# Kernel optimization log

Hardware: AMD Instinct MI355X
Metric: run time of the kernel (lower is better)

## Reference

```python
import jax, jax.numpy as jnp
import numpy as np

S, B, H = 2048, 1, 1024
N_HEADS = 16
HEAD_DIM = H // N_HEADS
E, K, F = 8, 2, 2048  # experts, top_k, ffn_hidden
EPS = 1e-5


def layernorm(x, w, b):
    mu = jnp.mean(x, axis=-1, keepdims=True)
    var = jnp.mean(jnp.square(x - mu), axis=-1, keepdims=True)
    return (x - mu) * jax.lax.rsqrt(var + EPS) * w + b


def setup_inputs() -> dict:
    key = jax.random.key(0)
    ks = jax.random.split(key, 8)
    std = 0.02
    return {
        "x": jax.random.normal(ks[0], (S, B, H), dtype=jnp.float32),
        "ln1_w": jnp.ones((H,), jnp.float32),
        "ln1_b": jnp.zeros((H,), jnp.float32),
        "in_proj_w": jax.random.normal(ks[1], (3 * H, H), jnp.float32) * std,
        "in_proj_b": jnp.zeros((3 * H,), jnp.float32),
        "out_proj_w": jax.random.normal(ks[2], (H, H), jnp.float32) * std,
        "out_proj_b": jnp.zeros((H,), jnp.float32),
        "ln2_w": jnp.ones((H,), jnp.float32),
        "ln2_b": jnp.zeros((H,), jnp.float32),
        "router_w": jax.random.normal(ks[3], (E, H), jnp.float32) * std,
        "w1": jax.random.normal(ks[4], (E, H, F), jnp.float32) * std,
        "w2": jax.random.normal(ks[5], (E, F, H), jnp.float32) * std,
    }


def reference(x, ln1_w, ln1_b, in_proj_w, in_proj_b, out_proj_w, out_proj_b,
              ln2_w, ln2_b, router_w, w1, w2):
    s, b, h = x.shape
    # ---- causal self-attention (nn.MultiheadAttention math) ----
    hn = layernorm(x, ln1_w, ln1_b)
    qkv = hn @ in_proj_w.T + in_proj_b          # [S,B,3H]
    q, k, v = jnp.split(qkv, 3, axis=-1)
    q = q.reshape(s, b, N_HEADS, HEAD_DIM)
    k = k.reshape(s, b, N_HEADS, HEAD_DIM)
    v = v.reshape(s, b, N_HEADS, HEAD_DIM)
    scores = jnp.einsum('sbnd,tbnd->bnst', q, k) / np.sqrt(HEAD_DIM)
    causal = jnp.tril(jnp.ones((s, s), bool))
    scores = jnp.where(causal[None, None], scores, -jnp.inf)
    probs = jax.nn.softmax(scores, axis=-1)
    attn = jnp.einsum('bnst,tbnd->sbnd', probs, v).reshape(s, b, h)
    attn = attn @ out_proj_w.T + out_proj_b
    x1 = x + attn
    # ---- dMoE FFN: router softmax -> top-k gates -> expert GELU MLP ----
    hn2 = layernorm(x1, ln2_w, ln2_b).reshape(s * b, h)   # tokens [T,H]
    logits = hn2 @ router_w.T                              # [T,E]
    rp = jax.nn.softmax(logits, axis=-1)
    topw, topi = jax.lax.top_k(rp, K)                      # [T,K]
    gates = jnp.sum(jax.nn.one_hot(topi, E, dtype=hn2.dtype) * topw[..., None], axis=1)  # [T,E]
    hmid = jax.nn.gelu(jnp.einsum('th,ehf->tef', hn2, w1), approximate=False)  # [T,E,F]
    y = jnp.einsum('tef,efh->th', hmid * gates[:, :, None], w2)                # [T,H]
    return x1 + y.reshape(s, b, h)
```

## Files before the change

### kernel.cpp

```cpp
#include <hip/hip_runtime.h>

#define SL 2048
#define HID 1024
#define NHEAD 16
#define HD 64
#define NEXP 8
#define FF 2048
#define MAXTILE 40
#define MAXROWS (MAXTILE * 128)
#define CPAD 32
#define BPITCH 36

typedef short bf16x8 __attribute__((ext_vector_type(8)));
typedef float f32x4 __attribute__((ext_vector_type(4)));
typedef unsigned u32x4 __attribute__((ext_vector_type(4)));

__device__ __forceinline__ unsigned short f2bf(float f) {
  unsigned u = __builtin_bit_cast(unsigned, f);
  u += 0x7fffu + ((u >> 16) & 1u);
  return (unsigned short)(u >> 16);
}

__device__ __forceinline__ void gload16(const void* g, void* l) {
  __builtin_amdgcn_global_load_lds((const __attribute__((address_space(1))) void*)g,
                                   (__attribute__((address_space(3))) void*)l,
                                   16, 0, 0);
}

__device__ __forceinline__ void xcd_remap(int& bx, int& by) {
  const int nx = gridDim.x;
  const int nwg = nx * gridDim.y;
  const int L = by * nx + bx;
  const int per = nwg >> 3;
  const int Lp = (L & 7) * per + (L >> 3);
  bx = Lp % nx;
  by = Lp / nx;
}

#define PIPE_WAIT(i, NT)                                                     \
  if ((i) == (NT) - 1)                                                       \
    asm volatile("s_waitcnt vmcnt(0) lgkmcnt(0)" ::: "memory");              \
  else                                                                       \
    asm volatile("s_waitcnt vmcnt(4) lgkmcnt(0)" ::: "memory");              \
  __builtin_amdgcn_s_barrier();

#define GEMM_FRAGS_MFMA(CC)                                                  \
  bf16x8 af[4], bfr[4];                                                      \
  _Pragma("unroll")                                                          \
  for (int mt = 0; mt < 4; mt++)                                             \
    af[mt] = *reinterpret_cast<const bf16x8*>(                               \
        &Asm[CC][(wm + mt * 16 + la) * 32 + lk]);                            \
  _Pragma("unroll")                                                          \
  for (int nt = 0; nt < 4; nt++)                                             \
    bfr[nt] = *reinterpret_cast<const bf16x8*>(                              \
        &Bsm[CC][(wn + nt * 16 + la) * 32 + lk]);                            \
  __builtin_amdgcn_s_setprio(1);                                             \
  _Pragma("unroll")                                                          \
  for (int mt = 0; mt < 4; mt++)                                             \
    _Pragma("unroll")                                                        \
    for (int nt = 0; nt < 4; nt++)                                           \
      acc[mt][nt] =                                                          \
          __builtin_amdgcn_mfma_f32_16x16x32_bf16(af[mt], bfr[nt], acc[mt][nt], 0, 0, 0); \
  __builtin_amdgcn_s_setprio(0);

#define PIPE_ROT()                                                           \
  cc = (cc == 2) ? 0 : cc + 1;                                               \
  cs = (cs == 2) ? 0 : cs + 1;

template <int MODE>
__global__ __launch_bounds__(256) void gemm_bt(
    const unsigned short* __restrict__ A, const unsigned short* __restrict__ Bt,
    int M, int N, int Kstride, int Kloop,
    const float* __restrict__ bias,
    float* __restrict__ outf,
    unsigned short* __restrict__ q_out, unsigned short* __restrict__ k_out,
    unsigned short* __restrict__ vt_out)
{
  __shared__ unsigned short Asm[3][128 * 32];
  __shared__ unsigned short Bsm[3][128 * 32];
  int bx = blockIdx.x, by = blockIdx.y;
  xcd_remap(bx, by);
  const int tid = threadIdx.x;
  const int wave = tid >> 6;
  const int lane = tid & 63;
  const int m0 = by * 128;
  const int n0 = bx * 128;
  const int koff = blockIdx.z * Kloop;
  const int wm = (wave >> 1) * 64;
  const int wn = (wave & 1) * 64;
  const int la = lane & 15;
  const int lk = (lane >> 4) * 8;

  f32x4 acc[4][4] = {};

  const int srow = tid >> 2;
  const int skoff = (tid & 3) * 8;
  const unsigned short* Ag = A + (size_t)(m0 + srow) * Kstride + koff + skoff;
  const unsigned short* Bg = Bt + (size_t)(n0 + srow) * Kstride + koff + skoff;

  auto stage = [&](int s, int k0) {
    gload16(Ag + k0, &Asm[s][wave * 512]);
    gload16(Ag + (size_t)64 * Kstride + k0, &Asm[s][2048 + wave * 512]);
    gload16(Bg + k0, &Bsm[s][wave * 512]);
    gload16(Bg + (size_t)64 * Kstride + k0, &Bsm[s][2048 + wave * 512]);
  };

  stage(0, 0);
  stage(1, 32);
  const int NT = Kloop >> 5;
  int cc = 0, cs = 2;
  for (int i = 0; i < NT; ++i) {
    PIPE_WAIT(i, NT)
    if (i + 2 < NT) stage(cs, (i + 2) << 5);
    GEMM_FRAGS_MFMA(cc)
    PIPE_ROT()
  }

  const int lg = lane >> 4;
#pragma unroll
  for (int mt = 0; mt < 4; mt++) {
#pragma unroll
    for (int nt = 0; nt < 4; nt++) {
#pragma unroll
      for (int r = 0; r < 4; r++) {
        const int row = m0 + wm + mt * 16 + lg * 4 + r;
        const int col = n0 + wn + nt * 16 + la;
        float v = acc[mt][nt][r];
        if (MODE == 0) {
          v += bias[col];
          const int hh = (col & 1023) >> 6;
          const int dd = col & 63;
          const unsigned short bv = f2bf(v);
          if (col < 1024)
            q_out[(size_t)hh * SL * HD + (size_t)row * HD + dd] = bv;
          else if (col < 2048)
            k_out[(size_t)hh * SL * HD + (size_t)row * HD + dd] = bv;
          else
            vt_out[(size_t)hh * HD * SL + (size_t)dd * SL + row] = bv;
        } else {
          outf[(size_t)blockIdx.z * SL * HID + (size_t)row * HID + col] = v;
        }
      }
    }
  }
}


__device__ __forceinline__ bf16x8 bfragB(const unsigned short* Bu, int n, int lk) {
  const uint2 lo = *reinterpret_cast<const uint2*>(&Bu[n * BPITCH + lk]);
  const uint2 hi = *reinterpret_cast<const uint2*>(&Bu[n * BPITCH + lk + 4]);
  u32x4 w; w[0] = lo.x; w[1] = lo.y; w[2] = hi.x; w[3] = hi.y;
  return __builtin_bit_cast(bf16x8, w);
}

#define MOE_FRAGS_MFMA(CC)                                                   \
  bf16x8 af[4], bfr[4];                                                      \
  _Pragma("unroll")                                                          \
  for (int mt = 0; mt < 4; mt++)                                             \
    af[mt] = *reinterpret_cast<const bf16x8*>(                               \
        &Asm[CC][(wm + mt * 16 + la) * 32 + lk]);                            \
  _Pragma("unroll")                                                          \
  for (int nt = 0; nt < 4; nt++)                                             \
    bfr[nt] = bfragB(BsmU[CC], wn + nt * 16 + la, lk);                       \
  __builtin_amdgcn_s_setprio(1);                                             \
  _Pragma("unroll")                                                          \
  for (int mt = 0; mt < 4; mt++)                                             \
    _Pragma("unroll")                                                        \
    for (int nt = 0; nt < 4; nt++)                                           \
      acc[mt][nt] =                                                          \
          __builtin_amdgcn_mfma_f32_16x16x32_bf16(af[mt], bfr[nt], acc[mt][nt], 0, 0, 0); \
  __builtin_amdgcn_s_setprio(0);

__global__ __launch_bounds__(256) void gemm_moe1(
    const unsigned short* __restrict__ A, const float* __restrict__ w1,
    const int* __restrict__ perm, const float* __restrict__ gateg,
    const int* __restrict__ texp, const int* __restrict__ trow,
    unsigned short* __restrict__ hmidg)
{
  __shared__ unsigned short Asm[2][128 * 32];
  __shared__ unsigned short BsmU[2][128 * BPITCH];
  int bx = blockIdx.x, by = blockIdx.y;
  xcd_remap(bx, by);
  const int e = texp[by];
  if (e < 0) return;
  const int row0 = trow[by];
  const int tid = threadIdx.x;
  const int wave = tid >> 6;
  const int lane = tid & 63;
  const int n0 = bx * 128;
  const int wm = (wave >> 1) * 64;
  const int wn = (wave & 1) * 64;
  const int la = lane & 15;
  const int lk = (lane >> 4) * 8;
  f32x4 acc[4][4] = {};

  const int srow = tid >> 2;
  const int skoff = (tid & 3) * 8;
  const int p0 = perm[row0 + srow];
  const int p1 = perm[row0 + 64 + srow];
  const unsigned short* Ag0 = A + (size_t)(p0 < 0 ? 0 : (p0 >> 1)) * HID + skoff;
  const unsigned short* Ag1 = A + (size_t)(p1 < 0 ? 0 : (p1 >> 1)) * HID + skoff;
  const float* Bf = w1 + (size_t)e * HID * FF + n0;
  const int sc = tid & 31;
  const int skr = tid >> 5;

  auto stageA = [&](int buf, int k0) {
    gload16(Ag0 + k0, &Asm[buf][wave * 512]);
    gload16(Ag1 + k0, &Asm[buf][2048 + wave * 512]);
  };
  auto stageB = [&](int buf, int k0) {
#pragma unroll
    for (int p = 0; p < 4; p++) {
      const int k = p * 8 + skr;
      const float* src = Bf + (size_t)(k0 + k) * FF + sc;
#pragma unroll
      for (int j = 0; j < 4; j++)
        BsmU[buf][(sc + 32 * j) * BPITCH + k] = f2bf(src[32 * j]);
    }
  };

  stageA(0, 0);
  stageB(0, 0);
  __syncthreads();
  int cur = 0;
  for (int k0 = 0; k0 < HID; k0 += 32) {
    if (k0 + 32 < HID) {
      stageA(cur ^ 1, k0 + 32);
      stageB(cur ^ 1, k0 + 32);
    }
    MOE_FRAGS_MFMA(cur)
    __syncthreads();
    cur ^= 1;
  }

  const int lg = lane >> 4;
#pragma unroll
  for (int mt = 0; mt < 4; mt++) {
    float gr[4];
#pragma unroll
    for (int r = 0; r < 4; r++) gr[r] = gateg[row0 + wm + mt * 16 + lg * 4 + r];
#pragma unroll
    for (int nt = 0; nt < 4; nt++) {
#pragma unroll
      for (int r = 0; r < 4; r++) {
        const int grow = row0 + wm + mt * 16 + lg * 4 + r;
        const int col = n0 + wn + nt * 16 + la;
        const float v = acc[mt][nt][r];
        const float g = 0.5f * v * (1.0f + erff(v * 0.70710678118f));
        hmidg[(size_t)grow * FF + col] = f2bf(g * gr[r]);
      }
    }
  }
}

__global__ __launch_bounds__(256) void gemm_moe2(
    const unsigned short* __restrict__ A, const float* __restrict__ w2,
    const int* __restrict__ perm,
    const int* __restrict__ texp, const int* __restrict__ trow,
    float* __restrict__ ybuf)
{
  __shared__ unsigned short Asm[2][128 * 32];
  __shared__ unsigned short BsmU[2][128 * BPITCH];
  int bx = blockIdx.x, by = blockIdx.y;
  xcd_remap(bx, by);
  const int e = texp[by];
  if (e < 0) return;
  const int row0 = trow[by];
  const int tid = threadIdx.x;
  const int wave = tid >> 6;
  const int lane = tid & 63;
  const int n0 = bx * 128;
  const int koff = blockIdx.z * (FF / 2);
  const int wm = (wave >> 1) * 64;
  const int wn = (wave & 1) * 64;
  const int la = lane & 15;
  const int lk = (lane >> 4) * 8;
  f32x4 acc[4][4] = {};

  const int srow = tid >> 2;
  const int skoff = (tid & 3) * 8;
  const unsigned short* Ag = A + (size_t)(row0 + srow) * FF + koff + skoff;
  const float* Bf = w2 + (size_t)e * FF * HID + (size_t)koff * HID + n0;
  const int sc = tid & 31;
  const int skr = tid >> 5;

  auto stageA = [&](int buf, int k0) {
    gload16(Ag + k0, &Asm[buf][wave * 512]);
    gload16(Ag + (size_t)64 * FF + k0, &Asm[buf][2048 + wave * 512]);
  };
  auto stageB = [&](int buf, int k0) {
#pragma unroll
    for (int p = 0; p < 4; p++) {
      const int k = p * 8 + skr;
      const float* src = Bf + (size_t)(k0 + k) * HID + sc;
#pragma unroll
      for (int j = 0; j < 4; j++)
        BsmU[buf][(sc + 32 * j) * BPITCH + k] = f2bf(src[32 * j]);
    }
  };

  stageA(0, 0);
  stageB(0, 0);
  __syncthreads();
  int cur = 0;
  for (int k0 = 0; k0 < FF / 2; k0 += 32) {
    if (k0 + 32 < FF / 2) {
      stageA(cur ^ 1, k0 + 32);
      stageB(cur ^ 1, k0 + 32);
    }
    MOE_FRAGS_MFMA(cur)
    __syncthreads();
    cur ^= 1;
  }

  const int lg = lane >> 4;
#pragma unroll
  for (int mt = 0; mt < 4; mt++) {
    int pr[4];
#pragma unroll
    for (int r = 0; r < 4; r++) pr[r] = perm[row0 + wm + mt * 16 + lg * 4 + r];
#pragma unroll
    for (int nt = 0; nt < 4; nt++) {
#pragma unroll
      for (int r = 0; r < 4; r++) {
        const int p = pr[r];
        if (p >= 0) {
          const int col = n0 + wn + nt * 16 + la;
          ybuf[(size_t)(blockIdx.z * 2 + (p & 1)) * SL * HID + (size_t)(p >> 1) * HID + col] =
              acc[mt][nt][r];
        }
      }
    }
  }
}

__global__ __launch_bounds__(256) void ln_kernel(
    const float* __restrict__ x, const float* __restrict__ w, const float* __restrict__ b,
    unsigned short* __restrict__ ob)
{
  const int row = blockIdx.x;
  const int tid = threadIdx.x;
  const float4 v = *reinterpret_cast<const float4*>(&x[(size_t)row * HID + tid * 4]);
  float s = v.x + v.y + v.z + v.w;
  float q = v.x * v.x + v.y * v.y + v.z * v.z + v.w * v.w;
  for (int off = 32; off > 0; off >>= 1) {
    s += __shfl_down(s, off);
    q += __shfl_down(q, off);
  }
  __shared__ float ps[4], pq[4];
  const int wave = tid >> 6, lane = tid & 63;
  if (lane == 0) { ps[wave] = s; pq[wave] = q; }
  __syncthreads();
  s = ps[0] + ps[1] + ps[2] + ps[3];
  q = pq[0] + pq[1] + pq[2] + pq[3];
  const float mu = s * (1.0f / HID);
  const float inv = rsqrtf(q * (1.0f / HID) - mu * mu + 1e-5f);
  const int i = tid * 4;
  const float4 wv = *reinterpret_cast<const float4*>(&w[i]);
  const float4 bv = *reinterpret_cast<const float4*>(&b[i]);
  ushort4 u;
  u.x = f2bf((v.x - mu) * inv * wv.x + bv.x);
  u.y = f2bf((v.y - mu) * inv * wv.y + bv.y);
  u.z = f2bf((v.z - mu) * inv * wv.z + bv.z);
  u.w = f2bf((v.w - mu) * inv * wv.w + bv.w);
  *reinterpret_cast<ushort4*>(&ob[(size_t)row * HID + i]) = u;
}

__global__ __launch_bounds__(256) void combine_ln(
    const float4* __restrict__ x, const float* __restrict__ bias,
    const float4* __restrict__ p0, const float4* __restrict__ p1,
    float4* __restrict__ x1,
    const float* __restrict__ w, const float* __restrict__ b,
    unsigned short* __restrict__ ob, float* __restrict__ of)
{
  const int row = blockIdx.x;
  const int tid = threadIdx.x;
  const int i4 = row * 256 + tid;
  const int i = tid * 4;
  const float4 bv0 = *reinterpret_cast<const float4*>(&bias[i]);
  const float4 a = x[i4], c = p0[i4], d = p1[i4];
  float4 v;
  v.x = a.x + bv0.x + c.x + d.x;
  v.y = a.y + bv0.y + c.y + d.y;
  v.z = a.z + bv0.z + c.z + d.z;
  v.w = a.w + bv0.w + c.w + d.w;
  x1[i4] = v;
  float s = v.x + v.y + v.z + v.w;
  float q = v.x * v.x + v.y * v.y + v.z * v.z + v.w * v.w;
  for (int off = 32; off > 0; off >>= 1) {
    s += __shfl_down(s, off);
    q += __shfl_down(q, off);
  }
  __shared__ float ps[4], pq[4];
  const int wave = tid >> 6, lane = tid & 63;
  if (lane == 0) { ps[wave] = s; pq[wave] = q; }
  __syncthreads();
  s = ps[0] + ps[1] + ps[2] + ps[3];
  q = pq[0] + pq[1] + pq[2] + pq[3];
  const float mu = s * (1.0f / HID);
  const float inv = rsqrtf(q * (1.0f / HID) - mu * mu + 1e-5f);
  const float4 wv = *reinterpret_cast<const float4*>(&w[i]);
  const float4 bv = *reinterpret_cast<const float4*>(&b[i]);
  const float o0 = (v.x - mu) * inv * wv.x + bv.x;
  const float o1 = (v.y - mu) * inv * wv.y + bv.y;
  const float o2 = (v.z - mu) * inv * wv.z + bv.z;
  const float o3 = (v.w - mu) * inv * wv.w + bv.w;
  ushort4 u; u.x = f2bf(o0); u.y = f2bf(o1); u.z = f2bf(o2); u.w = f2bf(o3);
  *reinterpret_cast<ushort4*>(&ob[(size_t)row * HID + i]) = u;
  float4 o; o.x = o0; o.y = o1; o.z = o2; o.w = o3;
  *reinterpret_cast<float4*>(&of[(size_t)row * HID + i]) = o;
}

__global__ __launch_bounds__(256) void conv_bf16_2(
    const float4* __restrict__ a, const float4* __restrict__ b,
    ushort4* __restrict__ oa, ushort4* __restrict__ ob, int na4, int nb4)
{
  const int i = blockIdx.x * 256 + threadIdx.x;
  if (i < na4) {
    const float4 v = a[i];
    ushort4 u; u.x = f2bf(v.x); u.y = f2bf(v.y); u.z = f2bf(v.z); u.w = f2bf(v.w);
    oa[i] = u;
  } else if (i - na4 < nb4) {
    const float4 v = b[i - na4];
    ushort4 u; u.x = f2bf(v.x); u.y = f2bf(v.y); u.z = f2bf(v.z); u.w = f2bf(v.w);
    ob[i - na4] = u;
  }
}

__global__ __launch_bounds__(256) void router_kernel(
    const float* __restrict__ hn2f, const float* __restrict__ rw,
    int* __restrict__ ti, float* __restrict__ tg, int* __restrict__ cnt)
{
  __shared__ float wlds[NEXP * HID];
  __shared__ int lcnt[NEXP];
  const int tid = threadIdx.x;
#pragma unroll
  for (int i = 0; i < 8; i++)
    *reinterpret_cast<float4*>(&wlds[i * 1024 + tid * 4]) =
        *reinterpret_cast<const float4*>(&rw[i * 1024 + tid * 4]);
  if (tid < NEXP) lcnt[tid] = 0;
  __syncthreads();

  const int wave = tid >> 6, lane = tid & 63;
#pragma unroll 1
  for (int k = 0; k < 4; k++) {
    const int t = blockIdx.x * 16 + wave * 4 + k;
    float4 xr[4];
#pragma unroll
    for (int c = 0; c < 4; c++)
      xr[c] = *reinterpret_cast<const float4*>(&hn2f[(size_t)t * HID + c * 256 + lane * 4]);
    float p[NEXP];
#pragma unroll
    for (int e = 0; e < NEXP; e++) {
      float s = 0.f;
#pragma unroll
      for (int c = 0; c < 4; c++) {
        const float4 wv = *reinterpret_cast<const float4*>(&wlds[e * 1024 + c * 256 + lane * 4]);
        s += xr[c].x * wv.x + xr[c].y * wv.y + xr[c].z * wv.z + xr[c].w * wv.w;
      }
      s += __shfl_xor(s, 32);
      s += __shfl_xor(s, 16);
      s += __shfl_xor(s, 8);
      s += __shfl_xor(s, 4);
      s += __shfl_xor(s, 2);
      s += __shfl_xor(s, 1);
      p[e] = s;
    }
    if (lane == 0) {
      float mx = p[0];
#pragma unroll
      for (int e = 1; e < NEXP; e++) mx = fmaxf(mx, p[e]);
      float Z = 0.f;
#pragma unroll
      for (int e = 0; e < NEXP; e++) { p[e] = expf(p[e] - mx); Z += p[e]; }
      const float invZ = 1.f / Z;
      int i1 = 0;
#pragma unroll
      for (int e = 1; e < NEXP; e++) if (p[e] > p[i1]) i1 = e;
      int i2 = (i1 == 0) ? 1 : 0;
#pragma unroll
      for (int e = 0; e < NEXP; e++) if (e != i1 && p[e] > p[i2]) i2 = e;
      ti[2 * t] = i1; ti[2 * t + 1] = i2;
      tg[2 * t] = p[i1] * invZ; tg[2 * t + 1] = p[i2] * invZ;
      atomicAdd(&lcnt[i1], 1);
      atomicAdd(&lcnt[i2], 1);
    }
  }
  __syncthreads();
  if (tid < NEXP && lcnt[tid] > 0) atomicAdd(&cnt[tid * CPAD], lcnt[tid]);
}

__global__ void scan_kernel(const int* __restrict__ cnt, int* __restrict__ poff,
                            int* __restrict__ texp, int* __restrict__ trow)
{
  if (threadIdx.x == 0 && blockIdx.x == 0) {
    int off = 0, nt = 0;
    for (int e = 0; e < NEXP; e++) {
      poff[e] = off;
      const int c = cnt[e * CPAD];
      const int ntl = (c + 127) >> 7;
      for (int i = 0; i < ntl; i++) { texp[nt] = e; trow[nt] = off + i * 128; nt++; }
      off += ntl * 128;
    }
    for (int i = nt; i < MAXTILE; i++) { texp[i] = -1; trow[i] = 0; }
  }
}

__global__ __launch_bounds__(256) void build_kernel(
    const int* __restrict__ ti, const float* __restrict__ tg,
    const int* __restrict__ poff, int* __restrict__ fill,
    int* __restrict__ perm, float* __restrict__ gateg)
{
  __shared__ int lcnt[NEXP], lbase[NEXP];
  const int tid = threadIdx.x;
  if (tid < NEXP) lcnt[tid] = 0;
  __syncthreads();
  const int t = blockIdx.x * 256 + tid;
  int e0 = ti[2 * t], e1 = ti[2 * t + 1];
  int l0 = atomicAdd(&lcnt[e0], 1);
  int l1 = atomicAdd(&lcnt[e1], 1);
  __syncthreads();
  if (tid < NEXP) lbase[tid] = (lcnt[tid] > 0) ? atomicAdd(&fill[tid * CPAD], lcnt[tid]) : 0;
  __syncthreads();
  int pos0 = poff[e0] + lbase[e0] + l0;
  int pos1 = poff[e1] + lbase[e1] + l1;
  perm[pos0] = 2 * t;
  gateg[pos0] = tg[2 * t];
  perm[pos1] = 2 * t + 1;
  gateg[pos1] = tg[2 * t + 1];
}

__global__ __launch_bounds__(256) void final_add(
    const float4* __restrict__ x1, const float4* __restrict__ y0,
    const float4* __restrict__ y1, const float4* __restrict__ y2,
    const float4* __restrict__ y3, float4* __restrict__ out)
{
  const int i = blockIdx.x * 256 + threadIdx.x;
  const float4 a = x1[i], b = y0[i], c = y1[i], d = y2[i], e = y3[i];
  float4 o;
  o.x = a.x + b.x + c.x + d.x + e.x;
  o.y = a.y + b.y + c.y + d.y + e.y;
  o.z = a.z + b.z + c.z + d.z + e.z;
  o.w = a.w + b.w + c.w + d.w + e.w;
  out[i] = o;
}

#define SC2 0.1803368801111204f
#define PPITCH 20
__global__ __launch_bounds__(512) void attn_kernel(
    const unsigned short* __restrict__ qb, const unsigned short* __restrict__ kb,
    const unsigned short* __restrict__ vtb, unsigned short* __restrict__ attn)
{
  const int h = blockIdx.y;
  const int tid = threadIdx.x;
  const int wave = tid >> 6, lane = tid & 63;
  const int grp = wave >> 2;
  const int w4 = wave & 3;
  const int la = lane & 15, lg = lane >> 4;
  const int la7 = la & 7;
  __shared__ unsigned short Kt[2][2][64 * 64];
  __shared__ unsigned short Vt[2][2][64 * 64];
  __shared__ unsigned plds[8 * 32 * PPITCH];
  const unsigned short* qh = qb + (size_t)h * SL * HD;
  const unsigned short* kh = kb + (size_t)h * SL * HD;
  const unsigned short* vh = vtb + (size_t)h * HD * SL;
  unsigned* pu = &plds[wave * 32 * PPITCH];

  const int sr_lo = w4 * 8 + (lane >> 3);
  const int ss = lane & 7;

  auto stageKV = [&](int t, int buf) {
    const int kvb = t * 64;
#pragma unroll
    for (int j = 0; j < 2; j++) {
      const int row = j * 32 + sr_lo;
      const int s = ss ^ (row & 7);
      gload16(kh + (size_t)(kvb + row) * HD + s * 8, &Kt[grp][buf][j * 2048 + w4 * 512]);
      gload16(vh + (size_t)row * SL + kvb + s * 8, &Vt[grp][buf][j * 2048 + w4 * 512]);
    }
  };

  for (int half = 0; half < 2; half++) {
    const int qt = half ? (31 - blockIdx.x) : blockIdx.x;
    const int m0 = qt * 64 + w4 * 16;
    const int T = qt + 1;
    const int S = (T + 1) >> 1;
    const int q = m0 + la;

    bf16x8 aq0 = *reinterpret_cast<const bf16x8*>(&qh[(size_t)(m0 + la) * HD + lg * 8]);
    bf16x8 aq1 = *reinterpret_cast<const bf16x8*>(&qh[(size_t)(m0 + la) * HD + 32 + lg * 8]);

    f32x4 oacc[4] = {};
    float mrun = -1e30f, lrun = 0.f;

    if (grp < T) stageKV(grp, 0);
    __syncthreads();
    int cur = 0;

    for (int s = 0; s < S; s++) {
      const int tmy = 2 * s + grp;
      if (tmy + 2 < T) stageKV(tmy + 2, cur ^ 1);
      if (tmy < T) {
        const int kv0 = tmy * 64;
        const unsigned short* Kb = Kt[grp][cur];
        const unsigned short* Vb = Vt[grp][cur];

        f32x4 sac[4] = {};
        __builtin_amdgcn_s_setprio(1);
#pragma unroll
        for (int nt = 0; nt < 4; nt++) {
          const int row = nt * 16 + la;
          bf16x8 b0 = *reinterpret_cast<const bf16x8*>(&Kb[row * 64 + ((lg ^ la7) << 3)]);
          bf16x8 b1 = *reinterpret_cast<const bf16x8*>(&Kb[row * 64 + (((4 + lg) ^ la7) << 3)]);
          sac[nt] = __builtin_amdgcn_mfma_f32_16x16x32_bf16(b0, aq0, sac[nt], 0, 0, 0);
          sac[nt] = __builtin_amdgcn_mfma_f32_16x16x32_bf16(b1, aq1, sac[nt], 0, 0, 0);
        }
        __builtin_amdgcn_s_setprio(0);
        float sv[4][4];
        const bool diag = (tmy == qt);
#pragma unroll
        for (int nt = 0; nt < 4; nt++)
#pragma unroll
          for (int r = 0; r < 4; r++) {
            float xs = sac[nt][r] * SC2;
            if (diag && (kv0 + nt * 16 + lg * 4 + r) > q) xs = -1e30f;
            sv[nt][r] = xs;
          }
        float pm = fmaxf(fmaxf(sv[0][0], sv[0][1]), fmaxf(sv[0][2], sv[0][3]));
#pragma unroll
        for (int nt = 1; nt < 4; nt++)
          pm = fmaxf(pm, fmaxf(fmaxf(sv[nt][0], sv[nt][1]), fmaxf(sv[nt][2], sv[nt][3])));
        pm = fmaxf(pm, __shfl_xor(pm, 16));
        pm = fmaxf(pm, __shfl_xor(pm, 32));
        const float mn = fmaxf(mrun, pm);
        float rs = 0.f;
#pragma unroll
        for (int nt = 0; nt < 4; nt++)
#pragma unroll
          for (int r = 0; r < 4; r++) {
            const float pe = exp2f(sv[nt][r] - mn);
            sv[nt][r] = pe;
            rs += pe;
          }
        rs += __shfl_xor(rs, 16);
        rs += __shfl_xor(rs, 32);
        if (__ballot(pm > mrun) != 0ULL) {
          const float al = exp2f(mrun - mn);
#pragma unroll
          for (int dt = 0; dt < 4; dt++)
#pragma unroll
            for (int r = 0; r < 4; r++) oacc[dt][r] *= al;
          lrun = lrun * al + rs;
          mrun = mn;
        } else {
          lrun += rs;
        }
#pragma unroll
        for (int nt = 0; nt < 4; nt++)
#pragma unroll
          for (int rp = 0; rp < 2; rp++) {
            unsigned pk;
            asm("v_cvt_pk_bf16_f32 %0, %1, %2"
                : "=v"(pk) : "v"(sv[nt][rp * 2]), "v"(sv[nt][rp * 2 + 1]));
            pu[(nt * 8 + lg * 2 + rp) * PPITCH + la] = pk;
          }
        asm volatile("s_waitcnt lgkmcnt(0)" ::: "memory");
        __builtin_amdgcn_sched_barrier(0);
        u32x4 w0, w1;
#pragma unroll
        for (int jj = 0; jj < 4; jj++) {
          w0[jj] = pu[(lg * 4 + jj) * PPITCH + la];
          w1[jj] = pu[(16 + lg * 4 + jj) * PPITCH + la];
        }
        const bf16x8 pa0 = __builtin_bit_cast(bf16x8, w0);
        const bf16x8 pa1 = __builtin_bit_cast(bf16x8, w1);
        __builtin_amdgcn_s_setprio(1);
#pragma unroll
        for (int dt = 0; dt < 4; dt++) {
          const int row = dt * 16 + la;
          bf16x8 v0 = *reinterpret_cast<const bf16x8*>(&Vb[row * 64 + ((lg ^ la7) << 3)]);
          bf16x8 v1 = *reinterpret_cast<const bf16x8*>(&Vb[row * 64 + (((4 + lg) ^ la7) << 3)]);
          oacc[dt] = __builtin_amdgcn_mfma_f32_16x16x32_bf16(v0, pa0, oacc[dt], 0, 0, 0);
          oacc[dt] = __builtin_amdgcn_mfma_f32_16x16x32_bf16(v1, pa1, oacc[dt], 0, 0, 0);
        }
        __builtin_amdgcn_s_setprio(0);
      }
      __syncthreads();
      cur ^= 1;
    }

    float* xb = (float*)&Kt[0][0][0];
    float* mlb = (float*)&Vt[0][0][0];
    if (grp == 1) {
#pragma unroll
      for (int dt = 0; dt < 4; dt++)
#pragma unroll
        for (int r = 0; r < 4; r++)
          xb[w4 * 1024 + (dt * 16 + lg * 4 + r) * 16 + la] = oacc[dt][r];
      if (lg == 0) {
        mlb[w4 * 32 + la * 2] = mrun;
        mlb[w4 * 32 + la * 2 + 1] = lrun;
      }
    }
    __syncthreads();
    if (grp == 0) {
      const float m1 = mlb[w4 * 32 + la * 2];
      const float l1 = mlb[w4 * 32 + la * 2 + 1];
      const float mm = fmaxf(mrun, m1);
      const float a0 = exp2f(mrun - mm);
      const float a1 = exp2f(m1 - mm);
      const float linv = 1.0f / (lrun * a0 + l1 * a1);
#pragma unroll
      for (int dt = 0; dt < 4; dt++) {
        ushort4 u;
        float o0 = (oacc[dt][0] * a0 + xb[w4 * 1024 + (dt * 16 + lg * 4 + 0) * 16 + la] * a1) * linv;
        float o1 = (oacc[dt][1] * a0 + xb[w4 * 1024 + (dt * 16 + lg * 4 + 1) * 16 + la] * a1) * linv;
        float o2 = (oacc[dt][2] * a0 + xb[w4 * 1024 + (dt * 16 + lg * 4 + 2) * 16 + la] * a1) * linv;
        float o3 = (oacc[dt][3] * a0 + xb[w4 * 1024 + (dt * 16 + lg * 4 + 3) * 16 + la] * a1) * linv;
        u.x = f2bf(o0); u.y = f2bf(o1); u.z = f2bf(o2); u.w = f2bf(o3);
        *reinterpret_cast<ushort4*>(&attn[(size_t)q * HID + h * HD + dt * 16 + lg * 4]) = u;
      }
    }
    __syncthreads();
  }
}

extern "C" void kernel_launch(void* const* d_in, const int* in_sizes, int n_in,
                              void* d_out, int out_size, void* d_ws, size_t ws_size,
                              hipStream_t stream)
{
  const float* x          = (const float*)d_in[0];
  const float* ln1_w      = (const float*)d_in[1];
  const float* ln1_b      = (const float*)d_in[2];
  const float* in_proj_w  = (const float*)d_in[3];
  const float* in_proj_b  = (const float*)d_in[4];
  const float* out_proj_w = (const float*)d_in[5];
  const float* out_proj_b = (const float*)d_in[6];
  const float* ln2_w      = (const float*)d_in[7];
  const float* ln2_b      = (const float*)d_in[8];
  const float* router_w   = (const float*)d_in[9];
  const float* w1         = (const float*)d_in[10];
  const float* w2         = (const float*)d_in[11];
  float* out = (float*)d_out;

  char* ws = (char*)d_ws;
  size_t off = 0;
  auto alloc = [&](size_t bytes) -> void* {
    void* p = ws + off;
    off += (bytes + 255) & ~(size_t)255;
    return p;
  };
  unsigned short* hn_b   = (unsigned short*)alloc((size_t)SL * HID * 2);
  unsigned short* ipw_b  = (unsigned short*)alloc((size_t)3 * HID * HID * 2);
  unsigned short* opw_b  = (unsigned short*)alloc((size_t)HID * HID * 2);
  unsigned short* qb     = (unsigned short*)alloc((size_t)SL * HID * 2);
  unsigned short* kb     = (unsigned short*)alloc((size_t)SL * HID * 2);
  unsigned short* vtb    = (unsigned short*)alloc((size_t)SL * HID * 2);
  unsigned short* attn_b = (unsigned short*)alloc((size_t)SL * HID * 2);
  float*          x1     = (float*)alloc((size_t)SL * HID * 4);
  float*          pbuf   = (float*)alloc((size_t)2 * SL * HID * 4);
  unsigned short* hn2_b  = (unsigned short*)alloc((size_t)SL * HID * 2);
  float*          hn2_f  = (float*)alloc((size_t)SL * HID * 4);
  unsigned short* hmidg  = (unsigned short*)alloc((size_t)MAXROWS * FF * 2);
  float*          ybuf   = (float*)alloc((size_t)4 * SL * HID * 4);
  int*            ti     = (int*)alloc((size_t)SL * 2 * 4);
  float*          tg     = (float*)alloc((size_t)SL * 2 * 4);
  int*            perm   = (int*)alloc((size_t)MAXROWS * 4);
  float*          gateg  = (float*)alloc((size_t)MAXROWS * 4);
  int*            cnt    = (int*)alloc(NEXP * CPAD * 4);
  int*            fill   = (int*)alloc(NEXP * CPAD * 4);
  int*            poff   = (int*)alloc(64 * 4);
  int*            texp   = (int*)alloc(64 * 4);
  int*            trow   = (int*)alloc(64 * 4);

  const dim3 blk(256);

  hipMemsetAsync(cnt, 0, NEXP * CPAD * 4, stream);
  hipMemsetAsync(fill, 0, NEXP * CPAD * 4, stream);
  hipMemsetAsync(perm, 0xFF, (size_t)MAXROWS * 4, stream);
  hipMemsetAsync(gateg, 0, (size_t)MAXROWS * 4, stream);

  conv_bf16_2<<<4096, blk, 0, stream>>>(
      (const float4*)in_proj_w, (const float4*)out_proj_w,
      (ushort4*)ipw_b, (ushort4*)opw_b, 3 * HID * HID / 4, HID * HID / 4);

  ln_kernel<<<SL, blk, 0, stream>>>(x, ln1_w, ln1_b, hn_b);

  gemm_bt<0><<<dim3(3 * HID / 128, SL / 128), blk, 0, stream>>>(
      hn_b, ipw_b, SL, 3 * HID, HID, HID,
      in_proj_b, nullptr, qb, kb, vtb);

  attn_kernel<<<dim3(16, NHEAD), dim3(512), 0, stream>>>(qb, kb, vtb, attn_b);

  gemm_bt<2><<<dim3(HID / 128, SL / 128, 2), blk, 0, stream>>>(
      attn_b, opw_b, SL, HID, HID, HID / 2,
      nullptr, pbuf, nullptr, nullptr, nullptr);

  combine_ln<<<SL, blk, 0, stream>>>(
      (const float4*)x, out_proj_b, (const float4*)pbuf,
      (const float4*)(pbuf + (size_t)SL * HID), (float4*)x1,
      ln2_w, ln2_b, hn2_b, hn2_f);

  router_kernel<<<SL / 16, blk, 0, stream>>>(hn2_f, router_w, ti, tg, cnt);
  scan_kernel<<<1, 64, 0, stream>>>(cnt, poff, texp, trow);
  build_kernel<<<SL / 256, blk, 0, stream>>>(ti, tg, poff, fill, perm, gateg);

  gemm_moe1<<<dim3(FF / 128, MAXTILE), blk, 0, stream>>>(
      hn2_b, w1, perm, gateg, texp, trow, hmidg);
  gemm_moe2<<<dim3(HID / 128, MAXTILE, 2), blk, 0, stream>>>(
      hmidg, w2, perm, texp, trow, ybuf);

  final_add<<<SL * HID / 1024, blk, 0, stream>>>(
      (const float4*)x1, (const float4*)ybuf,
      (const float4*)(ybuf + (size_t)SL * HID),
      (const float4*)(ybuf + (size_t)2 * SL * HID),
      (const float4*)(ybuf + (size_t)3 * SL * HID),
      (float4*)out);
}
```

Before: 261.2 us.

## Register-prefetch MoE weight tiles and give each attention block one query tile

Both MoE GEMM kernels now load the next fp32 weight tile into registers before the MFMA work and only convert and write it to LDS afterwards. This overlaps global-load latency with compute, at the cost of 16 extra registers and a full vmcnt wait. The attention kernel drops its two-query-tiles-per-block pairing and launches 32 blocks per head with one tile each, heaviest first. That doubles the block count for more parallelism but gives up the paired load balancing.

```diff
diff --git a/kernel.cpp b/kernel.cpp
--- a/kernel.cpp
+++ b/kernel.cpp
@@ -145,7 +145,6 @@
   }
 }
 
-
 __device__ __forceinline__ bf16x8 bfragB(const unsigned short* Bu, int n, int lk) {
   const uint2 lo = *reinterpret_cast<const uint2*>(&Bu[n * BPITCH + lk]);
   const uint2 hi = *reinterpret_cast<const uint2*>(&Bu[n * BPITCH + lk + 4]);
@@ -204,31 +203,44 @@
   const int sc = tid & 31;
   const int skr = tid >> 5;
 
+  float brg[16];
+
   auto stageA = [&](int buf, int k0) {
     gload16(Ag0 + k0, &Asm[buf][wave * 512]);
     gload16(Ag1 + k0, &Asm[buf][2048 + wave * 512]);
   };
-  auto stageB = [&](int buf, int k0) {
+  auto loadB = [&](int k0) {
+#pragma unroll
+    for (int p = 0; p < 4; p++) {
+      const float* src = Bf + (size_t)(k0 + p * 8 + skr) * FF + sc;
+#pragma unroll
+      for (int j = 0; j < 4; j++) brg[p * 4 + j] = src[32 * j];
+    }
+  };
+  auto writeB = [&](int buf) {
 #pragma unroll
     for (int p = 0; p < 4; p++) {
       const int k = p * 8 + skr;
-      const float* src = Bf + (size_t)(k0 + k) * FF + sc;
 #pragma unroll
       for (int j = 0; j < 4; j++)
-        BsmU[buf][(sc + 32 * j) * BPITCH + k] = f2bf(src[32 * j]);
+        BsmU[buf][(sc + 32 * j) * BPITCH + k] = f2bf(brg[p * 4 + j]);
     }
   };
 
+  loadB(0);
   stageA(0, 0);
-  stageB(0, 0);
+  asm volatile("s_waitcnt vmcnt(0)" ::: "memory");
+  writeB(0);
   __syncthreads();
   int cur = 0;
   for (int k0 = 0; k0 < HID; k0 += 32) {
-    if (k0 + 32 < HID) {
-      stageA(cur ^ 1, k0 + 32);
-      stageB(cur ^ 1, k0 + 32);
-    }
+    const bool nx = (k0 + 32 < HID);
+    if (nx) { loadB(k0 + 32); stageA(cur ^ 1, k0 + 32); }
     MOE_FRAGS_MFMA(cur)
+    if (nx) {
+      asm volatile("s_waitcnt vmcnt(0)" ::: "memory");
+      writeB(cur ^ 1);
+    }
     __syncthreads();
     cur ^= 1;
   }
@@ -284,31 +296,44 @@
   const int sc = tid & 31;
   const int skr = tid >> 5;
 
+  float brg[16];
+
   auto stageA = [&](int buf, int k0) {
     gload16(Ag + k0, &Asm[buf][wave * 512]);
     gload16(Ag + (size_t)64 * FF + k0, &Asm[buf][2048 + wave * 512]);
   };
-  auto stageB = [&](int buf, int k0) {
+  auto loadB = [&](int k0) {
+#pragma unroll
+    for (int p = 0; p < 4; p++) {
+      const float* src = Bf + (size_t)(k0 + p * 8 + skr) * HID + sc;
+#pragma unroll
+      for (int j = 0; j < 4; j++) brg[p * 4 + j] = src[32 * j];
+    }
+  };
+  auto writeB = [&](int buf) {
 #pragma unroll
     for (int p = 0; p < 4; p++) {
       const int k = p * 8 + skr;
-      const float* src = Bf + (size_t)(k0 + k) * HID + sc;
 #pragma unroll
       for (int j = 0; j < 4; j++)
-        BsmU[buf][(sc + 32 * j) * BPITCH + k] = f2bf(src[32 * j]);
+        BsmU[buf][(sc + 32 * j) * BPITCH + k] = f2bf(brg[p * 4 + j]);
     }
   };
 
+  loadB(0);
   stageA(0, 0);
-  stageB(0, 0);
+  asm volatile("s_waitcnt vmcnt(0)" ::: "memory");
+  writeB(0);
   __syncthreads();
   int cur = 0;
   for (int k0 = 0; k0 < FF / 2; k0 += 32) {
-    if (k0 + 32 < FF / 2) {
-      stageA(cur ^ 1, k0 + 32);
-      stageB(cur ^ 1, k0 + 32);
-    }
+    const bool nx = (k0 + 32 < FF / 2);
+    if (nx) { loadB(k0 + 32); stageA(cur ^ 1, k0 + 32); }
     MOE_FRAGS_MFMA(cur)
+    if (nx) {
+      asm volatile("s_waitcnt vmcnt(0)" ::: "memory");
+      writeB(cur ^ 1);
+    }
     __syncthreads();
     cur ^= 1;
   }
@@ -580,148 +605,145 @@
     }
   };
 
-  for (int half = 0; half < 2; half++) {
-    const int qt = half ? (31 - blockIdx.x) : blockIdx.x;
-    const int m0 = qt * 64 + w4 * 16;
-    const int T = qt + 1;
-    const int S = (T + 1) >> 1;
-    const int q = m0 + la;
-
-    bf16x8 aq0 = *reinterpret_cast<const bf16x8*>(&qh[(size_t)(m0 + la) * HD + lg * 8]);
-    bf16x8 aq1 = *reinterpret_cast<const bf16x8*>(&qh[(size_t)(m0 + la) * HD + 32 + lg * 8]);
-
-    f32x4 oacc[4] = {};
-    float mrun = -1e30f, lrun = 0.f;
-
-    if (grp < T) stageKV(grp, 0);
+  const int qt = 31 - (int)blockIdx.x;
+  const int m0 = qt * 64 + w4 * 16;
+  const int T = qt + 1;
+  const int S = (T + 1) >> 1;
+  const int q = m0 + la;
+
+  bf16x8 aq0 = *reinterpret_cast<const bf16x8*>(&qh[(size_t)(m0 + la) * HD + lg * 8]);
+  bf16x8 aq1 = *reinterpret_cast<const bf16x8*>(&qh[(size_t)(m0 + la) * HD + 32 + lg * 8]);
+
+  f32x4 oacc[4] = {};
+  float mrun = -1e30f, lrun = 0.f;
+
+  if (grp < T) stageKV(grp, 0);
+  __syncthreads();
+  int cur = 0;
+
+  for (int s = 0; s < S; s++) {
+    const int tmy = 2 * s + grp;
+    if (tmy + 2 < T) stageKV(tmy + 2, cur ^ 1);
+    if (tmy < T) {
+      const int kv0 = tmy * 64;
+      const unsigned short* Kb = Kt[grp][cur];
+      const unsigned short* Vb = Vt[grp][cur];
+
+      f32x4 sac[4] = {};
+      __builtin_amdgcn_s_setprio(1);
+#pragma unroll
+      for (int nt = 0; nt < 4; nt++) {
+        const int row = nt * 16 + la;
+        bf16x8 b0 = *reinterpret_cast<const bf16x8*>(&Kb[row * 64 + ((lg ^ la7) << 3)]);
+        bf16x8 b1 = *reinterpret_cast<const bf16x8*>(&Kb[row * 64 + (((4 + lg) ^ la7) << 3)]);
+        sac[nt] = __builtin_amdgcn_mfma_f32_16x16x32_bf16(b0, aq0, sac[nt], 0, 0, 0);
+        sac[nt] = __builtin_amdgcn_mfma_f32_16x16x32_bf16(b1, aq1, sac[nt], 0, 0, 0);
+      }
+      __builtin_amdgcn_s_setprio(0);
+      float sv[4][4];
+      const bool diag = (tmy == qt);
+#pragma unroll
+      for (int nt = 0; nt < 4; nt++)
+#pragma unroll
+        for (int r = 0; r < 4; r++) {
+          float xs = sac[nt][r] * SC2;
+          if (diag && (kv0 + nt * 16 + lg * 4 + r) > q) xs = -1e30f;
+          sv[nt][r] = xs;
+        }
+      float pm = fmaxf(fmaxf(sv[0][0], sv[0][1]), fmaxf(sv[0][2], sv[0][3]));
+#pragma unroll
+      for (int nt = 1; nt < 4; nt++)
+        pm = fmaxf(pm, fmaxf(fmaxf(sv[nt][0], sv[nt][1]), fmaxf(sv[nt][2], sv[nt][3])));
+      pm = fmaxf(pm, __shfl_xor(pm, 16));
+      pm = fmaxf(pm, __shfl_xor(pm, 32));
+      const float mn = fmaxf(mrun, pm);
+      float rs = 0.f;
+#pragma unroll
+      for (int nt = 0; nt < 4; nt++)
+#pragma unroll
+        for (int r = 0; r < 4; r++) {
+          const float pe = exp2f(sv[nt][r] - mn);
+          sv[nt][r] = pe;
+          rs += pe;
+        }
+      rs += __shfl_xor(rs, 16);
+      rs += __shfl_xor(rs, 32);
+      if (__ballot(pm > mrun) != 0ULL) {
+        const float al = exp2f(mrun - mn);
+#pragma unroll
+        for (int dt = 0; dt < 4; dt++)
+#pragma unroll
+          for (int r = 0; r < 4; r++) oacc[dt][r] *= al;
+        lrun = lrun * al + rs;
+        mrun = mn;
+      } else {
+        lrun += rs;
+      }
+#pragma unroll
+      for (int nt = 0; nt < 4; nt++)
+#pragma unroll
+        for (int rp = 0; rp < 2; rp++) {
+          unsigned pk;
+          asm("v_cvt_pk_bf16_f32 %0, %1, %2"
+              : "=v"(pk) : "v"(sv[nt][rp * 2]), "v"(sv[nt][rp * 2 + 1]));
+          pu[(nt * 8 + lg * 2 + rp) * PPITCH + la] = pk;
+        }
+      asm volatile("s_waitcnt lgkmcnt(0)" ::: "memory");
+      __builtin_amdgcn_sched_barrier(0);
+      u32x4 w0, w1;
+#pragma unroll
+      for (int jj = 0; jj < 4; jj++) {
+        w0[jj] = pu[(lg * 4 + jj) * PPITCH + la];
+        w1[jj] = pu[(16 + lg * 4 + jj) * PPITCH + la];
+      }
+      const bf16x8 pa0 = __builtin_bit_cast(bf16x8, w0);
+      const bf16x8 pa1 = __builtin_bit_cast(bf16x8, w1);
+      __builtin_amdgcn_s_setprio(1);
+#pragma unroll
+      for (int dt = 0; dt < 4; dt++) {
+        const int row = dt * 16 + la;
+        bf16x8 v0 = *reinterpret_cast<const bf16x8*>(&Vb[row * 64 + ((lg ^ la7) << 3)]);
+        bf16x8 v1 = *reinterpret_cast<const bf16x8*>(&Vb[row * 64 + (((4 + lg) ^ la7) << 3)]);
+        oacc[dt] = __builtin_amdgcn_mfma_f32_16x16x32_bf16(v0, pa0, oacc[dt], 0, 0, 0);
+        oacc[dt] = __builtin_amdgcn_mfma_f32_16x16x32_bf16(v1, pa1, oacc[dt], 0, 0, 0);
+      }
+      __builtin_amdgcn_s_setprio(0);
+    }
     __syncthreads();
-    int cur = 0;
-
-    for (int s = 0; s < S; s++) {
-      const int tmy = 2 * s + grp;
-      if (tmy + 2 < T) stageKV(tmy + 2, cur ^ 1);
-      if (tmy < T) {
-        const int kv0 = tmy * 64;
-        const unsigned short* Kb = Kt[grp][cur];
-        const unsigned short* Vb = Vt[grp][cur];
-
-        f32x4 sac[4] = {};
-        __builtin_amdgcn_s_setprio(1);
-#pragma unroll
-        for (int nt = 0; nt < 4; nt++) {
-          const int row = nt * 16 + la;
-          bf16x8 b0 = *reinterpret_cast<const bf16x8*>(&Kb[row * 64 + ((lg ^ la7) << 3)]);
-          bf16x8 b1 = *reinterpret_cast<const bf16x8*>(&Kb[row * 64 + (((4 + lg) ^ la7) << 3)]);
-          sac[nt] = __builtin_amdgcn_mfma_f32_16x16x32_bf16(b0, aq0, sac[nt], 0, 0, 0);
-          sac[nt] = __builtin_amdgcn_mfma_f32_16x16x32_bf16(b1, aq1, sac[nt], 0, 0, 0);
-        }
-        __builtin_amdgcn_s_setprio(0);
-        float sv[4][4];
-        const bool diag = (tmy == qt);
-#pragma unroll
-        for (int nt = 0; nt < 4; nt++)
-#pragma unroll
-          for (int r = 0; r < 4; r++) {
-            float xs = sac[nt][r] * SC2;
-            if (diag && (kv0 + nt * 16 + lg * 4 + r) > q) xs = -1e30f;
-            sv[nt][r] = xs;
-          }
-        float pm = fmaxf(fmaxf(sv[0][0], sv[0][1]), fmaxf(sv[0][2], sv[0][3]));
-#pragma unroll
-        for (int nt = 1; nt < 4; nt++)
-          pm = fmaxf(pm, fmaxf(fmaxf(sv[nt][0], sv[nt][1]), fmaxf(sv[nt][2], sv[nt][3])));
-        pm = fmaxf(pm, __shfl_xor(pm, 16));
-        pm = fmaxf(pm, __shfl_xor(pm, 32));
-        const float mn = fmaxf(mrun, pm);
-        float rs = 0.f;
-#pragma unroll
-        for (int nt = 0; nt < 4; nt++)
-#pragma unroll
-          for (int r = 0; r < 4; r++) {
-            const float pe = exp2f(sv[nt][r] - mn);
-            sv[nt][r] = pe;
-            rs += pe;
-          }
-        rs += __shfl_xor(rs, 16);
-        rs += __shfl_xor(rs, 32);
-        if (__ballot(pm > mrun) != 0ULL) {
-          const float al = exp2f(mrun - mn);
-#pragma unroll
-          for (int dt = 0; dt < 4; dt++)
-#pragma unroll
-            for (int r = 0; r < 4; r++) oacc[dt][r] *= al;
-          lrun = lrun * al + rs;
-          mrun = mn;
-        } else {
-          lrun += rs;
-        }
-#pragma unroll
-        for (int nt = 0; nt < 4; nt++)
-#pragma unroll
-          for (int rp = 0; rp < 2; rp++) {
-            unsigned pk;
-            asm("v_cvt_pk_bf16_f32 %0, %1, %2"
-                : "=v"(pk) : "v"(sv[nt][rp * 2]), "v"(sv[nt][rp * 2 + 1]));
-            pu[(nt * 8 + lg * 2 + rp) * PPITCH + la] = pk;
-          }
-        asm volatile("s_waitcnt lgkmcnt(0)" ::: "memory");
-        __builtin_amdgcn_sched_barrier(0);
-        u32x4 w0, w1;
-#pragma unroll
-        for (int jj = 0; jj < 4; jj++) {
-          w0[jj] = pu[(lg * 4 + jj) * PPITCH + la];
-          w1[jj] = pu[(16 + lg * 4 + jj) * PPITCH + la];
-        }
-        const bf16x8 pa0 = __builtin_bit_cast(bf16x8, w0);
-        const bf16x8 pa1 = __builtin_bit_cast(bf16x8, w1);
-        __builtin_amdgcn_s_setprio(1);
-#pragma unroll
-        for (int dt = 0; dt < 4; dt++) {
-          const int row = dt * 16 + la;
-          bf16x8 v0 = *reinterpret_cast<const bf16x8*>(&Vb[row * 64 + ((lg ^ la7) << 3)]);
-          bf16x8 v1 = *reinterpret_cast<const bf16x8*>(&Vb[row * 64 + (((4 + lg) ^ la7) << 3)]);
-          oacc[dt] = __builtin_amdgcn_mfma_f32_16x16x32_bf16(v0, pa0, oacc[dt], 0, 0, 0);
-          oacc[dt] = __builtin_amdgcn_mfma_f32_16x16x32_bf16(v1, pa1, oacc[dt], 0, 0, 0);
-        }
-        __builtin_amdgcn_s_setprio(0);
-      }
-      __syncthreads();
-      cur ^= 1;
-    }
-
-    float* xb = (float*)&Kt[0][0][0];
-    float* mlb = (float*)&Vt[0][0][0];
-    if (grp == 1) {
-#pragma unroll
-      for (int dt = 0; dt < 4; dt++)
-#pragma unroll
-        for (int r = 0; r < 4; r++)
-          xb[w4 * 1024 + (dt * 16 + lg * 4 + r) * 16 + la] = oacc[dt][r];
-      if (lg == 0) {
-        mlb[w4 * 32 + la * 2] = mrun;
-        mlb[w4 * 32 + la * 2 + 1] = lrun;
-      }
-    }
-    __syncthreads();
-    if (grp == 0) {
-      const float m1 = mlb[w4 * 32 + la * 2];
-      const float l1 = mlb[w4 * 32 + la * 2 + 1];
-      const float mm = fmaxf(mrun, m1);
-      const float a0 = exp2f(mrun - mm);
-      const float a1 = exp2f(m1 - mm);
-      const float linv = 1.0f / (lrun * a0 + l1 * a1);
-#pragma unroll
-      for (int dt = 0; dt < 4; dt++) {
-        ushort4 u;
-        float o0 = (oacc[dt][0] * a0 + xb[w4 * 1024 + (dt * 16 + lg * 4 + 0) * 16 + la] * a1) * linv;
-        float o1 = (oacc[dt][1] * a0 + xb[w4 * 1024 + (dt * 16 + lg * 4 + 1) * 16 + la] * a1) * linv;
-        float o2 = (oacc[dt][2] * a0 + xb[w4 * 1024 + (dt * 16 + lg * 4 + 2) * 16 + la] * a1) * linv;
-        float o3 = (oacc[dt][3] * a0 + xb[w4 * 1024 + (dt * 16 + lg * 4 + 3) * 16 + la] * a1) * linv;
-        u.x = f2bf(o0); u.y = f2bf(o1); u.z = f2bf(o2); u.w = f2bf(o3);
-        *reinterpret_cast<ushort4*>(&attn[(size_t)q * HID + h * HD + dt * 16 + lg * 4]) = u;
-      }
-    }
-    __syncthreads();
+    cur ^= 1;
+  }
+
+  float* xb = (float*)&Kt[0][0][0];
+  float* mlb = (float*)&Vt[0][0][0];
+  if (grp == 1) {
+#pragma unroll
+    for (int dt = 0; dt < 4; dt++)
+#pragma unroll
+      for (int r = 0; r < 4; r++)
+        xb[w4 * 1024 + (dt * 16 + lg * 4 + r) * 16 + la] = oacc[dt][r];
+    if (lg == 0) {
+      mlb[w4 * 32 + la * 2] = mrun;
+      mlb[w4 * 32 + la * 2 + 1] = lrun;
+    }
+  }
+  __syncthreads();
+  if (grp == 0) {
+    const float m1 = mlb[w4 * 32 + la * 2];
+    const float l1 = mlb[w4 * 32 + la * 2 + 1];
+    const float mm = fmaxf(mrun, m1);
+    const float a0 = exp2f(mrun - mm);
+    const float a1 = exp2f(m1 - mm);
+    const float linv = 1.0f / (lrun * a0 + l1 * a1);
+#pragma unroll
+    for (int dt = 0; dt < 4; dt++) {
+      ushort4 u;
+      float o0 = (oacc[dt][0] * a0 + xb[w4 * 1024 + (dt * 16 + lg * 4 + 0) * 16 + la] * a1) * linv;
+      float o1 = (oacc[dt][1] * a0 + xb[w4 * 1024 + (dt * 16 + lg * 4 + 1) * 16 + la] * a1) * linv;
+      float o2 = (oacc[dt][2] * a0 + xb[w4 * 1024 + (dt * 16 + lg * 4 + 2) * 16 + la] * a1) * linv;
+      float o3 = (oacc[dt][3] * a0 + xb[w4 * 1024 + (dt * 16 + lg * 4 + 3) * 16 + la] * a1) * linv;
+      u.x = f2bf(o0); u.y = f2bf(o1); u.z = f2bf(o2); u.w = f2bf(o3);
+      *reinterpret_cast<ushort4*>(&attn[(size_t)q * HID + h * HD + dt * 16 + lg * 4]) = u;
+    }
   }
 }
 
@@ -790,7 +812,7 @@
       hn_b, ipw_b, SL, 3 * HID, HID, HID,
       in_proj_b, nullptr, qb, kb, vtb);
 
-  attn_kernel<<<dim3(16, NHEAD), dim3(512), 0, stream>>>(qb, kb, vtb, attn_b);
+  attn_kernel<<<dim3(32, NHEAD), dim3(512), 0, stream>>>(qb, kb, vtb, attn_b);
 
   gemm_bt<2><<<dim3(HID / 128, SL / 128, 2), blk, 0, stream>>>(
       attn_b, opw_b, SL, HID, HID, HID / 2,
```

Result: slower. 286.9 us (+9.8%).
